# Kernel optimization log

Hardware: AMD Instinct MI355X
Metric: run time of the kernel (lower is better)

Reference implementation:

```python
import jax, jax.numpy as jnp
import numpy as np
import math

D_MODEL = 1024
N_HEAD = 16


def setup_inputs() -> dict:
    key = jax.random.key(0)
    ks = jax.random.split(key, 5)
    x = jax.random.normal(ks[0], (2, 2048, D_MODEL), dtype=jnp.float32)
    # Linear params (torch Linear: y = x @ W.T + b); store as [in, out] for einsum
    s1 = 1.0 / math.sqrt(D_MODEL)
    W_qkv = jax.random.uniform(ks[1], (D_MODEL, 3 * D_MODEL), jnp.float32, -s1, s1)
    b_qkv = jax.random.uniform(ks[2], (3 * D_MODEL,), jnp.float32, -s1, s1)
    W_out = jax.random.uniform(ks[3], (D_MODEL, D_MODEL), jnp.float32, -s1, s1)
    b_out = jax.random.uniform(ks[4], (D_MODEL,), jnp.float32, -s1, s1)
    return {"x": x, "W_qkv": W_qkv, "b_qkv": b_qkv, "W_out": W_out, "b_out": b_out}


def reference(x, W_qkv, b_qkv, W_out, b_out):
    B, L, D = x.shape
    H = N_HEAD
    hd = D // H
    qkv = x @ W_qkv + b_qkv                      # [B, L, 3D]
    q, k, v = jnp.split(qkv, 3, axis=-1)
    # [B, H, L, hd]
    q = q.reshape(B, L, H, hd).transpose(0, 2, 1, 3)
    k = k.reshape(B, L, H, hd).transpose(0, 2, 1, 3)
    v = v.reshape(B, L, H, hd).transpose(0, 2, 1, 3)
    scale = 1.0 / math.sqrt(hd)
    scores = jnp.einsum('bhqd,bhkd->bhqk', q, k) * scale   # [B, H, L, L]
    causal = jnp.tril(jnp.ones((L, L), dtype=bool))
    scores = jnp.where(causal, scores, jnp.float32(-jnp.inf))
    probs = jax.nn.softmax(scores, axis=-1)
    out = jnp.einsum('bhqk,bhkd->bhqd', probs, v)          # [B, H, L, hd]
    out = out.transpose(0, 2, 1, 3).reshape(B, L, D)
    out = out @ W_out + b_out
    return jnp.squeeze(out)
```

## Files before the change

kernel.cpp:

```cpp
#include <hip/hip_runtime.h>
#include <hip/hip_bf16.h>

#define SEQ    2048
#define NHEAD  16
#define HD     64
#define DMODEL 1024

using bf16 = __hip_bfloat16;
using short8 = __attribute__((ext_vector_type(8))) short;
using short4v = __attribute__((ext_vector_type(4))) short;
using f32x4  = __attribute__((ext_vector_type(4))) float;

__device__ __forceinline__ float fast_exp2(float x) {
  return __builtin_amdgcn_exp2f(x);
}
#define WAIT_LGKM0() __builtin_amdgcn_s_waitcnt(0xC07F)

__device__ __forceinline__ void gload_lds16(const bf16* g, bf16* l) {
  __builtin_amdgcn_global_load_lds(
      (const __attribute__((address_space(1))) void*)g,
      (__attribute__((address_space(3))) void*)l, 16, 0, 0);
}


__global__ void prep_k(const float* __restrict__ x, bf16* __restrict__ xb,
                       const float* __restrict__ Wqkv, bf16* __restrict__ WqkvT,
                       const float* __restrict__ Wout, bf16* __restrict__ WoutT) {
  __shared__ bf16 tile[32][33];
  const int id = blockIdx.x, tid = threadIdx.x;
  if (id < 2048) {
    int i = (id * 256 + tid) * 8;
    bf16 tmp[8];
    #pragma unroll
    for (int j = 0; j < 8; ++j) tmp[j] = __float2bfloat16(x[i + j]);
    *(short8*)&xb[i] = *(short8*)tmp;
    return;
  }
  const float* in; bf16* out; int R, C, tx32, ty32;
  if (id < 2048 + 3072) {
    int t = id - 2048; in = Wqkv; out = WqkvT; R = 1024; C = 3072;
    tx32 = t % 96; ty32 = t / 96;
  } else {
    int t = id - 5120; in = Wout; out = WoutT; R = 1024; C = 1024;
    tx32 = t % 32; ty32 = t / 32;
  }
  int c0 = tx32 * 32, r0 = ty32 * 32;
  int tx = tid & 31, ty = tid >> 5;
  #pragma unroll
  for (int i = ty; i < 32; i += 8)
    tile[i][tx] = __float2bfloat16(in[(size_t)(r0 + i) * C + c0 + tx]);
  __syncthreads();
  #pragma unroll
  for (int i = ty; i < 32; i += 8)
    out[(size_t)(c0 + i) * R + r0 + tx] = tile[tx][i];
}

__global__ void transpose_v_k(const bf16* __restrict__ in, bf16* __restrict__ out) {
  __shared__ bf16 tile[32][33];
  const int bh = blockIdx.z;
  const bf16* ip = in  + (size_t)bh * SEQ * HD;
  bf16* op       = out + (size_t)bh * HD * SEQ;
  int c0 = blockIdx.x * 32, r0 = blockIdx.y * 32;
  int tx = threadIdx.x & 31, ty = threadIdx.x >> 5;
  #pragma unroll
  for (int i = ty; i < 32; i += 8)
    tile[i][tx] = ip[(size_t)(r0 + i) * HD + c0 + tx];
  __syncthreads();
  #pragma unroll
  for (int i = ty; i < 32; i += 8)
    op[(size_t)(c0 + i) * SEQ + r0 + tx] = tile[tx][i];
}

template <int MODE>
__global__ __launch_bounds__(256)
void gemm_bt(const bf16* __restrict__ A, const bf16* __restrict__ BT,
             const float* __restrict__ bias,
             bf16* __restrict__ out0, bf16* __restrict__ out1,
             bf16* __restrict__ out2, float* __restrict__ outf) {
  constexpr int K = 1024;
  __shared__ __align__(16) bf16 As[128 * 32];
  __shared__ __align__(16) bf16 Bs[128 * 32];
  const int tid = threadIdx.x;
  const int wave = tid >> 6, lane = tid & 63;
  const int quad = lane >> 4, l16 = lane & 15;
  const int waveM = (wave >> 1) * 64, waveN = (wave & 1) * 64;
  const int m0 = blockIdx.x * 128, n0 = blockIdx.y * 128;
  const int srow = (lane >> 2);
  const int scol = (((lane & 3) ^ ((lane >> 3) & 3)) * 8);
  const int q8   = (quad ^ ((l16 >> 1) & 3)) * 8;

  const f32x4 zero4 = {0.f, 0.f, 0.f, 0.f};
  f32x4 acc[4][4];
  #pragma unroll
  for (int i = 0; i < 4; ++i)
    #pragma unroll
    for (int j = 0; j < 4; ++j) acc[i][j] = zero4;

  for (int k0 = 0; k0 < K; k0 += 32) {
    __syncthreads();
    #pragma unroll
    for (int half = 0; half < 2; ++half) {
      int grow = half * 64 + wave * 16 + srow;
      gload_lds16(&A [(size_t)(m0 + grow) * K + k0 + scol],
                  &As[(half * 64 + wave * 16) * 32]);
      gload_lds16(&BT[(size_t)(n0 + grow) * K + k0 + scol],
                  &Bs[(half * 64 + wave * 16) * 32]);
    }
    __syncthreads();
    short8 af[4], bfm[4];
    #pragma unroll
    for (int mt = 0; mt < 4; ++mt)
      af[mt] = *(const short8*)&As[(waveM + mt * 16 + l16) * 32 + q8];
    #pragma unroll
    for (int nt = 0; nt < 4; ++nt)
      bfm[nt] = *(const short8*)&Bs[(waveN + nt * 16 + l16) * 32 + q8];
    #pragma unroll
    for (int mt = 0; mt < 4; ++mt)
      #pragma unroll
      for (int nt = 0; nt < 4; ++nt)
        acc[mt][nt] = __builtin_amdgcn_mfma_f32_16x16x32_bf16(
            af[mt], bfm[nt], acc[mt][nt], 0, 0, 0);
  }

  #pragma unroll
  for (int nt = 0; nt < 4; ++nt) {
    int n = n0 + waveN + nt * 16 + l16;
    float bvv = bias[n];
    #pragma unroll
    for (int mt = 0; mt < 4; ++mt) {
      #pragma unroll
      for (int r = 0; r < 4; ++r) {
        int m = m0 + waveM + mt * 16 + quad * 4 + r;
        float v = acc[mt][nt][r] + bvv;
        if (MODE == 1) {
          outf[(size_t)m * 1024 + n] = v;
        } else {
          bf16 v16 = __float2bfloat16(v);
          int which = n >> 10, oo = n & 1023;
          int h = oo >> 6, c = oo & 63;
          int b = m >> 11, l = m & 2047;
          size_t idx = ((size_t)(b * NHEAD + h) * SEQ + l) * HD + c;
          if (which == 0)      out0[idx] = v16;
          else if (which == 1) out1[idx] = v16;
          else                 out2[idx] = v16;
        }
      }
    }
  }
}

__global__ __launch_bounds__(256)
void attn_k(const bf16* __restrict__ Q, const bf16* __restrict__ Kb,
            const bf16* __restrict__ VT, bf16* __restrict__ O) {
  __shared__ __align__(16) bf16 Ks[2][128 * 32];
  __shared__ __align__(16) bf16 Vs[4][64 * 32];
  __shared__ __align__(16) bf16 Plds[4][16][136];
  const int tid = threadIdx.x;
  const int wave = tid >> 6, lane = tid & 63;
  const int quad = lane >> 4, l16 = lane & 15;
  const int srow = lane >> 2;
  const int scol = (((lane & 3) ^ ((lane >> 3) & 3)) * 8);
  const int q8   = (quad ^ ((l16 >> 1) & 3)) * 8;
  const int id = blockIdx.x;
  const int bh = id & 31, blkx = id >> 5;
  const int b = bh >> 4, h = bh & 15;

  const bf16* Qp = Q  + (size_t)bh * SEQ * HD;
  const bf16* Kp = Kb + (size_t)bh * SEQ * HD;
  const bf16* Vp = VT + (size_t)bh * HD * SEQ;

  const f32x4 zero4 = {0.f, 0.f, 0.f, 0.f};
  const float c = 0.18033688011112042f;
  const float mc = 8.0f * c;

  for (int pass = 0; pass < 2; ++pass) {
    const int qt = pass ? (31 - blkx) : blkx;
    const int q0w = qt * 64 + wave * 16;
    const int q_lane = q0w + l16;
    const int ntiles = (qt + 2) >> 1;

    short8 qf0 = *(const short8*)&Qp[(size_t)(q0w + l16) * HD + quad * 8];
    short8 qf1 = *(const short8*)&Qp[(size_t)(q0w + l16) * HD + 32 + quad * 8];

    f32x4 oacc[4];
    #pragma unroll
    for (int dt = 0; dt < 4; ++dt) oacc[dt] = zero4;
    float l4[4] = {0.f, 0.f, 0.f, 0.f};

    for (int t = 0; t < ntiles; ++t) {
      const int k0 = t << 7;
      __syncthreads();
      #pragma unroll
      for (int i = 0; i < 2; ++i)
        #pragma unroll
        for (int hh = 0; hh < 2; ++hh)
          gload_lds16(&Kp[(size_t)(k0 + wave * 32 + i * 16 + srow) * HD + hh * 32 + scol],
                      &Ks[hh][(wave * 32 + i * 16) * 32]);
      #pragma unroll
      for (int g = 0; g < 4; ++g)
        gload_lds16(&Vp[(size_t)(g * 16 + srow) * SEQ + k0 + wave * 32 + scol],
                    &Vs[wave][(g * 16) * 32]);
      __syncthreads();

      f32x4 s[8];
      #pragma unroll
      for (int g = 0; g < 8; ++g) {
        short8 ka = *(const short8*)&Ks[0][(g * 16 + l16) * 32 + q8];
        short8 kb = *(const short8*)&Ks[1][(g * 16 + l16) * 32 + q8];
        f32x4 sg = zero4;
        sg = __builtin_amdgcn_mfma_f32_16x16x32_bf16(ka, qf0, sg, 0, 0, 0);
        sg = __builtin_amdgcn_mfma_f32_16x16x32_bf16(kb, qf1, sg, 0, 0, 0);
        s[g] = sg;
      }

      if (t == ntiles - 1) {
        #pragma unroll
        for (int g = 0; g < 8; ++g)
          #pragma unroll
          for (int r = 0; r < 4; ++r) {
            int k = k0 + g * 16 + quad * 4 + r;
            s[g][r] = (k <= q_lane) ? s[g][r] : -__builtin_inff();
          }
      }

      #pragma unroll
      for (int g = 0; g < 8; ++g) {
        bf16 pb[4];
        #pragma unroll
        for (int r = 0; r < 4; ++r) {
          float p = fast_exp2(__builtin_fmaf(s[g][r], c, -mc));
          l4[r] += p;
          pb[r] = __float2bfloat16(p);
        }
        *(short4v*)&Plds[wave][l16][g * 16 + quad * 4] = *(short4v*)pb;
      }
      WAIT_LGKM0();

      short8 pf[4];
      #pragma unroll
      for (int ch = 0; ch < 4; ++ch)
        pf[ch] = *(const short8*)&Plds[wave][l16][ch * 32 + quad * 8];
      #pragma unroll
      for (int ch = 0; ch < 4; ++ch)
        #pragma unroll
        for (int dt = 0; dt < 4; ++dt) {
          short8 vf = *(const short8*)&Vs[ch][(dt * 16 + l16) * 32 + q8];
          oacc[dt] = __builtin_amdgcn_mfma_f32_16x16x32_bf16(vf, pf[ch], oacc[dt], 0, 0, 0);
        }
    }

    float l_i = (l4[0] + l4[1]) + (l4[2] + l4[3]);
    l_i += __shfl_xor(l_i, 16, 64);
    l_i += __shfl_xor(l_i, 32, 64);
    float inv = 1.f / l_i;

    #pragma unroll
    for (int dt = 0; dt < 4; ++dt) {
      bf16 ob[4];
      #pragma unroll
      for (int r = 0; r < 4; ++r) ob[r] = __float2bfloat16(oacc[dt][r] * inv);
      *(short4v*)&Plds[wave][l16][dt * 16 + quad * 4] = *(short4v*)ob;
    }
    WAIT_LGKM0();
    {
      int row = lane >> 2;
      int col = (lane & 3) * 16;
      short8 o0 = *(const short8*)&Plds[wave][row][col];
      short8 o1 = *(const short8*)&Plds[wave][row][col + 8];
      size_t base = ((size_t)(b * SEQ + q0w + row)) * DMODEL + h * HD + col;
      *(short8*)&O[base]     = o0;
      *(short8*)&O[base + 8] = o1;
    }
    WAIT_LGKM0();
  }
}

extern "C" void kernel_launch(void* const* d_in, const int* in_sizes, int n_in,
                              void* d_out, int out_size, void* d_ws, size_t ws_size,
                              hipStream_t stream) {
  const float* x    = (const float*)d_in[0];
  const float* Wqkv = (const float*)d_in[1];
  const float* bqkv = (const float*)d_in[2];
  const float* Wout = (const float*)d_in[3];
  const float* bout = (const float*)d_in[4];
  float* out = (float*)d_out;

  char* ws = (char*)d_ws;
  const size_t MB = 1024 * 1024;
  char* big    = ws + 16384;
  bf16* Kbuf   = (bf16*)(big);
  bf16* VTb    = (bf16*)(big + 8 * MB);
  bf16* xb     = (bf16*)(big + 16 * MB);
  bf16* AO     = (bf16*)(big + 16 * MB);
  bf16* WqkvT  = (bf16*)(big + 24 * MB);
  bf16* WoutT  = (bf16*)(big + 30 * MB);
  bf16* Qb     = (bf16*)d_out;
  bf16* Vtmp   = (bf16*)((char*)d_out + 8 * MB);

  prep_k<<<6144, 256, 0, stream>>>(x, xb, Wqkv, WqkvT, Wout, WoutT);
  gemm_bt<0><<<dim3(4096 / 128, 3072 / 128), 256, 0, stream>>>(
      xb, WqkvT, bqkv, Qb, Kbuf, Vtmp, nullptr);
  transpose_v_k<<<dim3(HD / 32, SEQ / 32, 32), 256, 0, stream>>>(Vtmp, VTb);
  attn_k<<<512, 256, 0, stream>>>(Qb, Kbuf, VTb, AO);
  gemm_bt<1><<<dim3(4096 / 128, 1024 / 128), 256, 0, stream>>>(
      AO, WoutT, bout, nullptr, nullptr, nullptr, out);
}
```

Baseline: 181.1 us.

## Double-buffer K/V tiles in attention and shrink key tile to 64

The attention loop now prefetches the next K/V tile into a second LDS buffer while computing on the current one, with one barrier per iteration instead of two. The key tile shrinks from 128 to 64, so the causal diagonal wastes less masked work and LDS use per buffer falls. The cost is twice as many loop iterations and barriers, and less MFMA work per tile available to hide load latency.

Result: no change. 179.1 us (-1.1%).

```diff
diff --git a/kernel.cpp b/kernel.cpp
--- a/kernel.cpp
+++ b/kernel.cpp
@@ -152,9 +152,9 @@
 __global__ __launch_bounds__(256)
 void attn_k(const bf16* __restrict__ Q, const bf16* __restrict__ Kb,
             const bf16* __restrict__ VT, bf16* __restrict__ O) {
-  __shared__ __align__(16) bf16 Ks[2][128 * 32];
-  __shared__ __align__(16) bf16 Vs[4][64 * 32];
-  __shared__ __align__(16) bf16 Plds[4][16][136];
+  __shared__ __align__(16) bf16 Ks[2][2][64 * 32];
+  __shared__ __align__(16) bf16 Vs[2][2][64 * 32];
+  __shared__ __align__(16) bf16 Plds[4][16][72];
   const int tid = threadIdx.x;
   const int wave = tid >> 6, lane = tid & 63;
   const int quad = lane >> 4, l16 = lane & 15;
@@ -177,7 +177,7 @@
     const int qt = pass ? (31 - blkx) : blkx;
     const int q0w = qt * 64 + wave * 16;
     const int q_lane = q0w + l16;
-    const int ntiles = (qt + 2) >> 1;
+    const int ntiles = qt + 1;
 
     short8 qf0 = *(const short8*)&Qp[(size_t)(q0w + l16) * HD + quad * 8];
     short8 qf1 = *(const short8*)&Qp[(size_t)(q0w + l16) * HD + 32 + quad * 8];
@@ -187,26 +187,40 @@
     for (int dt = 0; dt < 4; ++dt) oacc[dt] = zero4;
     float l4[4] = {0.f, 0.f, 0.f, 0.f};
 
+
+    {
+      const int k0 = 0;
+      #pragma unroll
+      for (int hh = 0; hh < 2; ++hh)
+        gload_lds16(&Kp[(size_t)(k0 + wave * 16 + srow) * HD + hh * 32 + scol],
+                    &Ks[0][hh][(wave * 16) * 32]);
+      #pragma unroll
+      for (int ch = 0; ch < 2; ++ch)
+        gload_lds16(&Vp[(size_t)(wave * 16 + srow) * SEQ + k0 + ch * 32 + scol],
+                    &Vs[0][ch][(wave * 16) * 32]);
+    }
+    __syncthreads();
+
     for (int t = 0; t < ntiles; ++t) {
-      const int k0 = t << 7;
-      __syncthreads();
-      #pragma unroll
-      for (int i = 0; i < 2; ++i)
+      const int buf = t & 1;
+      if (t + 1 < ntiles) {
+        const int k1 = (t + 1) << 6, nb = buf ^ 1;
         #pragma unroll
         for (int hh = 0; hh < 2; ++hh)
-          gload_lds16(&Kp[(size_t)(k0 + wave * 32 + i * 16 + srow) * HD + hh * 32 + scol],
-                      &Ks[hh][(wave * 32 + i * 16) * 32]);
-      #pragma unroll
-      for (int g = 0; g < 4; ++g)
-        gload_lds16(&Vp[(size_t)(g * 16 + srow) * SEQ + k0 + wave * 32 + scol],
-                    &Vs[wave][(g * 16) * 32]);
-      __syncthreads();
-
-      f32x4 s[8];
-      #pragma unroll
-      for (int g = 0; g < 8; ++g) {
-        short8 ka = *(const short8*)&Ks[0][(g * 16 + l16) * 32 + q8];
-        short8 kb = *(const short8*)&Ks[1][(g * 16 + l16) * 32 + q8];
+          gload_lds16(&Kp[(size_t)(k1 + wave * 16 + srow) * HD + hh * 32 + scol],
+                      &Ks[nb][hh][(wave * 16) * 32]);
+        #pragma unroll
+        for (int ch = 0; ch < 2; ++ch)
+          gload_lds16(&Vp[(size_t)(wave * 16 + srow) * SEQ + k1 + ch * 32 + scol],
+                      &Vs[nb][ch][(wave * 16) * 32]);
+      }
+      const int k0 = t << 6;
+
+      f32x4 s[4];
+      #pragma unroll
+      for (int g = 0; g < 4; ++g) {
+        short8 ka = *(const short8*)&Ks[buf][0][(g * 16 + l16) * 32 + q8];
+        short8 kb = *(const short8*)&Ks[buf][1][(g * 16 + l16) * 32 + q8];
         f32x4 sg = zero4;
         sg = __builtin_amdgcn_mfma_f32_16x16x32_bf16(ka, qf0, sg, 0, 0, 0);
         sg = __builtin_amdgcn_mfma_f32_16x16x32_bf16(kb, qf1, sg, 0, 0, 0);
@@ -215,7 +229,7 @@
 
       if (t == ntiles - 1) {
         #pragma unroll
-        for (int g = 0; g < 8; ++g)
+        for (int g = 0; g < 4; ++g)
           #pragma unroll
           for (int r = 0; r < 4; ++r) {
             int k = k0 + g * 16 + quad * 4 + r;
@@ -224,7 +238,7 @@
       }
 
       #pragma unroll
-      for (int g = 0; g < 8; ++g) {
+      for (int g = 0; g < 4; ++g) {
         bf16 pb[4];
         #pragma unroll
         for (int r = 0; r < 4; ++r) {
@@ -236,17 +250,16 @@
       }
       WAIT_LGKM0();
 
-      short8 pf[4];
-      #pragma unroll
-      for (int ch = 0; ch < 4; ++ch)
-        pf[ch] = *(const short8*)&Plds[wave][l16][ch * 32 + quad * 8];
-      #pragma unroll
-      for (int ch = 0; ch < 4; ++ch)
+      #pragma unroll
+      for (int ch = 0; ch < 2; ++ch) {
+        short8 pf = *(const short8*)&Plds[wave][l16][ch * 32 + quad * 8];
         #pragma unroll
         for (int dt = 0; dt < 4; ++dt) {
-          short8 vf = *(const short8*)&Vs[ch][(dt * 16 + l16) * 32 + q8];
-          oacc[dt] = __builtin_amdgcn_mfma_f32_16x16x32_bf16(vf, pf[ch], oacc[dt], 0, 0, 0);
+          short8 vf = *(const short8*)&Vs[buf][ch][(dt * 16 + l16) * 32 + q8];
+          oacc[dt] = __builtin_amdgcn_mfma_f32_16x16x32_bf16(vf, pf, oacc[dt], 0, 0, 0);
         }
+      }
+      __syncthreads();
     }
 
     float l_i = (l4[0] + l4[1]) + (l4[2] + l4[3]);
```
